# Kernel optimization log

Hardware: AMD Instinct MI355X
Metric: run time of the kernel (lower is better)

## Reference

```python
import jax, jax.numpy as jnp
import numpy as np

M0 = 0.3
R = 2
H = W = 64  # grid size from init_kwargs
N = H * W
B = 2


def _make_grid():
    # grid_by(lims=[[1,-1],[-1,1]], size=(64,64)): cartesian_prod of the two
    # linspaces, then columns swapped via index_select([1, 0]).
    a = jnp.linspace(1.0, -1.0, H)
    b = jnp.linspace(-1.0, 1.0, W)
    ga, gb = jnp.meshgrid(a, b, indexing='ij')
    cart = jnp.stack([ga, gb], axis=-1).reshape(N, 2)  # cartesian_prod order
    return cart[:, ::-1]  # swap columns -> [N, 2]


def setup_inputs() -> dict:
    key = jax.random.key(0)
    k1, k2 = jax.random.split(key)
    grid = _make_grid()
    # input points = grid + small jitter (avoids exactly-zero distances)
    inp = grid[None, :, :] + 0.05 * jax.random.normal(k1, (B, N, 2), dtype=jnp.float32)
    weight = jax.random.uniform(k2, (B, N), dtype=jnp.float32)
    return {"input": inp, "weight": weight, "grid": grid}


def reference(input, weight, grid):
    # --- brute-force KNN (r=2), k = N (full sort; equivalent to torch max_k path) ---
    # dist[b, j, i] = || grid_j - input_{b,i} ||_2   (note the .mT in torch knn)
    d2 = jnp.sum((grid[None, :, None, :] - input[:, None, :, :]) ** 2, axis=-1)  # [B,N,N]
    dist = jnp.sqrt(d2)
    order = jnp.argsort(dist, axis=-1)                       # ascending distance
    knn_dist = jnp.take_along_axis(dist, order, axis=-1)     # [B,N,N]
    knn_index = order                                        # indices into input points

    # --- weighted DTM ---
    weight_bound = M0 * jnp.sum(weight, axis=-1, keepdims=True)   # [B,1]
    wb = weight_bound[:, :, None]                                  # [B,1,1]
    # gather per-row weights of the sorted neighbors
    knn_weight = jax.vmap(lambda w, idx: w[idx])(weight, knn_index)  # [B,N,N]
    cum_knn_weight = jnp.cumsum(knn_weight, axis=-1)
    # searchsorted (left): first index where cumulative weight >= bound
    k_index = jnp.sum(cum_knn_weight < wb, axis=-1, keepdims=True)   # [B,N,1]
    k_index = jnp.minimum(k_index, N - 1)

    r_dist = knn_dist ** 2  # r == 2
    cum_dist = jnp.cumsum(r_dist * knn_weight, axis=-1)
    dtm_val = jnp.take_along_axis(
        cum_dist + r_dist * (wb - cum_knn_weight), k_index, axis=-1
    ).squeeze(-1)                                                    # [B,N]
    return jnp.sqrt(dtm_val / weight_bound)
```

## Files before the change

### kernel.cpp

```cpp
#include <hip/hip_runtime.h>
#include <math.h>

namespace {

constexpr int   kN       = 4096;
constexpr int   kThreads = 256;
constexpr int   kEPT     = kN / 64;
constexpr int   kGroups  = kEPT / 2;
constexpr int   kIters   = 9;
constexpr float kM0      = 0.3f;
constexpr float kS       = 2048.f;
constexpr float kRootS   = 45.25483399593904f;

typedef _Float16 h2 __attribute__((ext_vector_type(2)));

__device__ __forceinline__ float dppStep_(float x, int t) {
    return x + __builtin_bit_cast(float, t);
}
__device__ __forceinline__ float waveSumUniform(float x) {
    int xi;
    xi = __builtin_amdgcn_update_dpp(0, __builtin_bit_cast(int, x), 0x111, 0xf, 0xf, true);
    x  = dppStep_(x, xi);
    xi = __builtin_amdgcn_update_dpp(0, __builtin_bit_cast(int, x), 0x112, 0xf, 0xf, true);
    x  = dppStep_(x, xi);
    xi = __builtin_amdgcn_update_dpp(0, __builtin_bit_cast(int, x), 0x114, 0xf, 0xf, true);
    x  = dppStep_(x, xi);
    xi = __builtin_amdgcn_update_dpp(0, __builtin_bit_cast(int, x), 0x118, 0xf, 0xf, true);
    x  = dppStep_(x, xi);
    xi = __builtin_amdgcn_update_dpp(0, __builtin_bit_cast(int, x), 0x142, 0xa, 0xf, true);
    x  = dppStep_(x, xi);
    xi = __builtin_amdgcn_update_dpp(0, __builtin_bit_cast(int, x), 0x143, 0xc, 0xf, true);
    x  = dppStep_(x, xi);
    return __builtin_bit_cast(float, __builtin_amdgcn_readlane(__builtin_bit_cast(int, x), 63));
}

__device__ __forceinline__ h2 subClamp(h2 m, h2 d) {
    h2 r;
    asm("v_pk_add_f16 %0, %1, %2 neg_lo:[0,1] neg_hi:[0,1] clamp"
        : "=v"(r) : "v"(m), "v"(d));
    return r;
}

__global__ __launch_bounds__(kThreads, 4)
void dtm_kernel(const float* __restrict__ input,
                const float* __restrict__ weight,
                const float* __restrict__ grid,
                float* __restrict__ out,
                int nq) {
    const int lane = threadIdx.x & 63;
    const int wave = threadIdx.x >> 6;
    const int wglob = blockIdx.x * 4 + wave;
    const int b    = wglob >> 11;
    const int wid  = wglob & 2047;
    const int i0 = wid;
    const int i1 = wid + kN / 2;
    if (b * kN + i1 >= nq) return;

    const float sgxA = kRootS * grid[2 * i0], sgyA = kRootS * grid[2 * i0 + 1];
    const float sgxB = kRootS * grid[2 * i1], sgyB = kRootS * grid[2 * i1 + 1];
    const float4* inp4 = (const float4*)(input + (size_t)b * kN * 2);
    const float4* wgt4 = (const float4*)(weight + (size_t)b * kN);

    const h2 one2 = h2{(_Float16)1.f, (_Float16)1.f};

    h2 dA[kGroups], dB[kGroups], ws[kGroups];
    float wl = 0.f;
#pragma unroll
    for (int s = 0; s < kGroups / 2; ++s) {
        const int g = lane + 64 * s;
        const float4 wv = wgt4[g];
        const float4 pa = inp4[2 * g];
        const float4 pb = inp4[2 * g + 1];
        float dx, dy, e0, e1, e2, e3;
        dx = fmaf(-kRootS, pa.x, sgxA); dy = fmaf(-kRootS, pa.y, sgyA); e0 = fmaf(dy, dy, dx * dx);
        dx = fmaf(-kRootS, pa.z, sgxA); dy = fmaf(-kRootS, pa.w, sgyA); e1 = fmaf(dy, dy, dx * dx);
        dx = fmaf(-kRootS, pb.x, sgxA); dy = fmaf(-kRootS, pb.y, sgyA); e2 = fmaf(dy, dy, dx * dx);
        dx = fmaf(-kRootS, pb.z, sgxA); dy = fmaf(-kRootS, pb.w, sgyA); e3 = fmaf(dy, dy, dx * dx);
        dA[2 * s]     = h2{(_Float16)e0, (_Float16)e1};
        dA[2 * s + 1] = h2{(_Float16)e2, (_Float16)e3};
        dx = fmaf(-kRootS, pa.x, sgxB); dy = fmaf(-kRootS, pa.y, sgyB); e0 = fmaf(dy, dy, dx * dx);
        dx = fmaf(-kRootS, pa.z, sgxB); dy = fmaf(-kRootS, pa.w, sgyB); e1 = fmaf(dy, dy, dx * dx);
        dx = fmaf(-kRootS, pb.x, sgxB); dy = fmaf(-kRootS, pb.y, sgyB); e2 = fmaf(dy, dy, dx * dx);
        dx = fmaf(-kRootS, pb.z, sgxB); dy = fmaf(-kRootS, pb.w, sgyB); e3 = fmaf(dy, dy, dx * dx);
        dB[2 * s]     = h2{(_Float16)e0, (_Float16)e1};
        dB[2 * s + 1] = h2{(_Float16)e2, (_Float16)e3};
        ws[2 * s]     = h2{(_Float16)wv.x, (_Float16)wv.y};
        ws[2 * s + 1] = h2{(_Float16)wv.z, (_Float16)wv.w};
        wl = __builtin_amdgcn_fdot2(ws[2 * s],     one2, wl, false);
        wl = __builtin_amdgcn_fdot2(ws[2 * s + 1], one2, wl, false);
    }
    const float wb = kM0 * waveSumUniform(wl);

    float loA = 0.f, hiA = 32768.f, TloA = 0.f;
    float loB = 0.f, hiB = 32768.f, TloB = 0.f;
#pragma unroll 1
    for (int it = 0; it < kIters; ++it) {
        const float midA = 0.5f * (loA + hiA);
        const float midB = 0.5f * (loB + hiB);
        const _Float16 mAh = (_Float16)midA;
        const _Float16 mBh = (_Float16)midB;
        const h2 mA2 = h2{mAh, mAh};
        const h2 mB2 = h2{mBh, mBh};
        float a0 = 0.f, a1 = 0.f, b0 = 0.f, b1 = 0.f;
#pragma unroll
        for (int g = 0; g < kGroups; g += 2) {
            h2 tA0 = subClamp(mA2, dA[g]);
            h2 tA1 = subClamp(mA2, dA[g + 1]);
            h2 tB0 = subClamp(mB2, dB[g]);
            h2 tB1 = subClamp(mB2, dB[g + 1]);
            a0 = __builtin_amdgcn_fdot2(ws[g],     tA0, a0, false);
            a1 = __builtin_amdgcn_fdot2(ws[g + 1], tA1, a1, false);
            b0 = __builtin_amdgcn_fdot2(ws[g],     tB0, b0, false);
            b1 = __builtin_amdgcn_fdot2(ws[g + 1], tB1, b1, false);
        }
        const float TA = waveSumUniform(a0 + a1);
        const float TB = waveSumUniform(b0 + b1);
        if (TA >= wb) hiA = midA; else { loA = midA; TloA = TA; }
        if (TB >= wb) hiB = midB; else { loB = midB; TloB = TB; }
    }

    {
        const _Float16 lAh = (_Float16)loA;
        const _Float16 lBh = (_Float16)loB;
        const h2 lA2 = h2{lAh, lAh};
        const h2 lB2 = h2{lBh, lBh};
        float A0 = 0.f, A1 = 0.f, B0 = 0.f, B1 = 0.f;
#pragma unroll
        for (int g = 0; g < kGroups; g += 2) {
            const h2 tA0 = subClamp(lA2, dA[g]);
            const h2 tA1 = subClamp(lA2, dA[g + 1]);
            const h2 tB0 = subClamp(lB2, dB[g]);
            const h2 tB1 = subClamp(lB2, dB[g + 1]);
            const h2 pA0 = dA[g] * ws[g];
            const h2 pA1 = dA[g + 1] * ws[g + 1];
            const h2 pB0 = dB[g] * ws[g];
            const h2 pB1 = dB[g + 1] * ws[g + 1];
            A0 = __builtin_amdgcn_fdot2(pA0, tA0, A0, false);
            A1 = __builtin_amdgcn_fdot2(pA1, tA1, A1, false);
            B0 = __builtin_amdgcn_fdot2(pB0, tB0, B0, false);
            B1 = __builtin_amdgcn_fdot2(pB1, tB1, B1, false);
        }
        const float AA = waveSumUniform(A0 + A1);
        const float AB = waveSumUniform(B0 + B1);
        if (lane == 0) {
            const float dtmA = (AA + hiA * (wb - TloA)) * (1.f / kS);
            const float dtmB = (AB + hiB * (wb - TloB)) * (1.f / kS);
            float* ob = out + (size_t)b * kN;
            ob[i0] = sqrtf(fmaxf(dtmA, 0.f) / wb);
            ob[i1] = sqrtf(fmaxf(dtmB, 0.f) / wb);
        }
    }
}

}

extern "C" void kernel_launch(void* const* d_in, const int* in_sizes, int n_in,
                              void* d_out, int out_size, void* d_ws, size_t ws_size,
                              hipStream_t stream) {
    const float* input  = (const float*)d_in[0];
    const float* weight = (const float*)d_in[1];
    const float* grid   = (const float*)d_in[2];
    float* out = (float*)d_out;
    const int nq = out_size;
    const int blocks = (nq + 7) / 8;
    dtm_kernel<<<dim3(blocks), dim3(kThreads), 0, stream>>>(input, weight, grid, out, nq);
}
```

Baseline: 75.39 us.

## Seed bisection with an asymmetric split and adaptively stop refinement iterations

The bisection search for the threshold now begins with one evaluation at a seed value of 4096, which splits the range unevenly. It then runs 6 fixed iterations, followed by up to 3 extra iterations that run only while an interval is still wider than about 64, so uniform waves can exit early. The distance setup also switches to packed f32 FMA inline assembly, processing both query points per instruction. The aim is fewer full passes over the 64 fp16 distance registers per wave, at the cost of more branching and a possible accuracy difference when the seed lands badly.

Result: no change. 74.13 us (-1.7%).

```diff
diff --git a/kernel.cpp b/kernel.cpp
--- a/kernel.cpp
+++ b/kernel.cpp
@@ -3,16 +3,19 @@
 
 namespace {
 
-constexpr int   kN       = 4096;
-constexpr int   kThreads = 256;
-constexpr int   kEPT     = kN / 64;
-constexpr int   kGroups  = kEPT / 2;
-constexpr int   kIters   = 9;
-constexpr float kM0      = 0.3f;
-constexpr float kS       = 2048.f;
-constexpr float kRootS   = 45.25483399593904f;
+constexpr int   kN         = 4096;
+constexpr int   kThreads   = 256;
+constexpr int   kGroups    = 32;
+constexpr int   kItersMain = 6;
+constexpr float kM0        = 0.3f;
+constexpr float kS         = 2048.f;
+constexpr float kRootS     = 45.25483399593904f;
+constexpr float kSeed      = 4096.f;
+constexpr float kTop       = 32768.f;
 
 typedef _Float16 h2 __attribute__((ext_vector_type(2)));
+typedef float    f2 __attribute__((ext_vector_type(2)));
+typedef float    f4 __attribute__((ext_vector_type(4)));
 
 __device__ __forceinline__ float dppStep_(float x, int t) {
     return x + __builtin_bit_cast(float, t);
@@ -39,6 +42,44 @@
     asm("v_pk_add_f16 %0, %1, %2 neg_lo:[0,1] neg_hi:[0,1] clamp"
         : "=v"(r) : "v"(m), "v"(d));
     return r;
+}
+
+__device__ __forceinline__ f2 pk_fma_bx(f2 a, f2 p, f2 c) {
+    f2 d;
+    asm("v_pk_fma_f32 %0, %1, %2, %3 op_sel_hi:[1,0,1]"
+        : "=v"(d) : "v"(a), "v"(p), "v"(c));
+    return d;
+}
+__device__ __forceinline__ f2 pk_fma_by(f2 a, f2 p, f2 c) {
+    f2 d;
+    asm("v_pk_fma_f32 %0, %1, %2, %3 op_sel:[0,1,0] op_sel_hi:[1,1,1]"
+        : "=v"(d) : "v"(a), "v"(p), "v"(c));
+    return d;
+}
+__device__ __forceinline__ f2 pk_mul(f2 a, f2 b) {
+    f2 d; asm("v_pk_mul_f32 %0, %1, %2" : "=v"(d) : "v"(a), "v"(b)); return d;
+}
+__device__ __forceinline__ f2 pk_fma(f2 a, f2 b, f2 c) {
+    f2 d; asm("v_pk_fma_f32 %0, %1, %2, %3" : "=v"(d) : "v"(a), "v"(b), "v"(c)); return d;
+}
+
+__device__ __forceinline__ void evalT(const h2 (&dA)[kGroups], const h2 (&dB)[kGroups],
+                                      const h2 (&ws)[kGroups], h2 mA2, h2 mB2,
+                                      float& TA, float& TB) {
+    float a0 = 0.f, a1 = 0.f, b0 = 0.f, b1 = 0.f;
+#pragma unroll
+    for (int g = 0; g < kGroups; g += 2) {
+        h2 tA0 = subClamp(mA2, dA[g]);
+        h2 tA1 = subClamp(mA2, dA[g + 1]);
+        h2 tB0 = subClamp(mB2, dB[g]);
+        h2 tB1 = subClamp(mB2, dB[g + 1]);
+        a0 = __builtin_amdgcn_fdot2(ws[g],     tA0, a0, false);
+        a1 = __builtin_amdgcn_fdot2(ws[g + 1], tA1, a1, false);
+        b0 = __builtin_amdgcn_fdot2(ws[g],     tB0, b0, false);
+        b1 = __builtin_amdgcn_fdot2(ws[g + 1], tB1, b1, false);
+    }
+    TA = waveSumUniform(a0 + a1);
+    TB = waveSumUniform(b0 + b1);
 }
 
 __global__ __launch_bounds__(kThreads, 4)
@@ -58,65 +99,84 @@
 
     const float sgxA = kRootS * grid[2 * i0], sgyA = kRootS * grid[2 * i0 + 1];
     const float sgxB = kRootS * grid[2 * i1], sgyB = kRootS * grid[2 * i1 + 1];
-    const float4* inp4 = (const float4*)(input + (size_t)b * kN * 2);
-    const float4* wgt4 = (const float4*)(weight + (size_t)b * kN);
-
-    const h2 one2 = h2{(_Float16)1.f, (_Float16)1.f};
+    const f4* inp4 = (const f4*)(input + (size_t)b * kN * 2);
+    const f4* wgt4 = (const f4*)(weight + (size_t)b * kN);
+
+    const h2 one2  = h2{(_Float16)1.f, (_Float16)1.f};
+    const f2 negr2 = f2{-kRootS, -kRootS};
+    const f2 sgx2  = f2{sgxA, sgxB};
+    const f2 sgy2  = f2{sgyA, sgyB};
 
     h2 dA[kGroups], dB[kGroups], ws[kGroups];
     float wl = 0.f;
 #pragma unroll
     for (int s = 0; s < kGroups / 2; ++s) {
         const int g = lane + 64 * s;
-        const float4 wv = wgt4[g];
-        const float4 pa = inp4[2 * g];
-        const float4 pb = inp4[2 * g + 1];
-        float dx, dy, e0, e1, e2, e3;
-        dx = fmaf(-kRootS, pa.x, sgxA); dy = fmaf(-kRootS, pa.y, sgyA); e0 = fmaf(dy, dy, dx * dx);
-        dx = fmaf(-kRootS, pa.z, sgxA); dy = fmaf(-kRootS, pa.w, sgyA); e1 = fmaf(dy, dy, dx * dx);
-        dx = fmaf(-kRootS, pb.x, sgxA); dy = fmaf(-kRootS, pb.y, sgyA); e2 = fmaf(dy, dy, dx * dx);
-        dx = fmaf(-kRootS, pb.z, sgxA); dy = fmaf(-kRootS, pb.w, sgyA); e3 = fmaf(dy, dy, dx * dx);
-        dA[2 * s]     = h2{(_Float16)e0, (_Float16)e1};
-        dA[2 * s + 1] = h2{(_Float16)e2, (_Float16)e3};
-        dx = fmaf(-kRootS, pa.x, sgxB); dy = fmaf(-kRootS, pa.y, sgyB); e0 = fmaf(dy, dy, dx * dx);
-        dx = fmaf(-kRootS, pa.z, sgxB); dy = fmaf(-kRootS, pa.w, sgyB); e1 = fmaf(dy, dy, dx * dx);
-        dx = fmaf(-kRootS, pb.x, sgxB); dy = fmaf(-kRootS, pb.y, sgyB); e2 = fmaf(dy, dy, dx * dx);
-        dx = fmaf(-kRootS, pb.z, sgxB); dy = fmaf(-kRootS, pb.w, sgyB); e3 = fmaf(dy, dy, dx * dx);
-        dB[2 * s]     = h2{(_Float16)e0, (_Float16)e1};
-        dB[2 * s + 1] = h2{(_Float16)e2, (_Float16)e3};
-        ws[2 * s]     = h2{(_Float16)wv.x, (_Float16)wv.y};
-        ws[2 * s + 1] = h2{(_Float16)wv.z, (_Float16)wv.w};
+        const f4 wv  = wgt4[g];
+        const f4 pa4 = inp4[2 * g];
+        const f4 pb4 = inp4[2 * g + 1];
+        const f2 p0 = __builtin_shufflevector(pa4, pa4, 0, 1);
+        const f2 p1 = __builtin_shufflevector(pa4, pa4, 2, 3);
+        const f2 p2 = __builtin_shufflevector(pb4, pb4, 0, 1);
+        const f2 p3 = __builtin_shufflevector(pb4, pb4, 2, 3);
+        f2 dx, dy, q0, q1, q2, q3;
+        dx = pk_fma_bx(negr2, p0, sgx2); dy = pk_fma_by(negr2, p0, sgy2);
+        q0 = pk_fma(dy, dy, pk_mul(dx, dx));
+        dx = pk_fma_bx(negr2, p1, sgx2); dy = pk_fma_by(negr2, p1, sgy2);
+        q1 = pk_fma(dy, dy, pk_mul(dx, dx));
+        dx = pk_fma_bx(negr2, p2, sgx2); dy = pk_fma_by(negr2, p2, sgy2);
+        q2 = pk_fma(dy, dy, pk_mul(dx, dx));
+        dx = pk_fma_bx(negr2, p3, sgx2); dy = pk_fma_by(negr2, p3, sgy2);
+        q3 = pk_fma(dy, dy, pk_mul(dx, dx));
+        dA[2 * s]     = h2{(_Float16)q0[0], (_Float16)q1[0]};
+        dA[2 * s + 1] = h2{(_Float16)q2[0], (_Float16)q3[0]};
+        dB[2 * s]     = h2{(_Float16)q0[1], (_Float16)q1[1]};
+        dB[2 * s + 1] = h2{(_Float16)q2[1], (_Float16)q3[1]};
+        ws[2 * s]     = h2{(_Float16)wv[0], (_Float16)wv[1]};
+        ws[2 * s + 1] = h2{(_Float16)wv[2], (_Float16)wv[3]};
         wl = __builtin_amdgcn_fdot2(ws[2 * s],     one2, wl, false);
         wl = __builtin_amdgcn_fdot2(ws[2 * s + 1], one2, wl, false);
     }
     const float wb = kM0 * waveSumUniform(wl);
 
-    float loA = 0.f, hiA = 32768.f, TloA = 0.f;
-    float loB = 0.f, hiB = 32768.f, TloB = 0.f;
+    float loA, hiA, TloA, loB, hiB, TloB;
+    {
+        const _Float16 sh = (_Float16)kSeed;
+        const h2 s2 = h2{sh, sh};
+        float TA, TB;
+        evalT(dA, dB, ws, s2, s2, TA, TB);
+        if (TA >= wb) { loA = 0.f;   hiA = kSeed; TloA = 0.f; }
+        else          { loA = kSeed; hiA = kTop;  TloA = TA;  }
+        if (TB >= wb) { loB = 0.f;   hiB = kSeed; TloB = 0.f; }
+        else          { loB = kSeed; hiB = kTop;  TloB = TB;  }
+    }
+
 #pragma unroll 1
-    for (int it = 0; it < kIters; ++it) {
+    for (int it = 0; it < kItersMain; ++it) {
         const float midA = 0.5f * (loA + hiA);
         const float midB = 0.5f * (loB + hiB);
         const _Float16 mAh = (_Float16)midA;
         const _Float16 mBh = (_Float16)midB;
-        const h2 mA2 = h2{mAh, mAh};
-        const h2 mB2 = h2{mBh, mBh};
-        float a0 = 0.f, a1 = 0.f, b0 = 0.f, b1 = 0.f;
-#pragma unroll
-        for (int g = 0; g < kGroups; g += 2) {
-            h2 tA0 = subClamp(mA2, dA[g]);
-            h2 tA1 = subClamp(mA2, dA[g + 1]);
-            h2 tB0 = subClamp(mB2, dB[g]);
-            h2 tB1 = subClamp(mB2, dB[g + 1]);
-            a0 = __builtin_amdgcn_fdot2(ws[g],     tA0, a0, false);
-            a1 = __builtin_amdgcn_fdot2(ws[g + 1], tA1, a1, false);
-            b0 = __builtin_amdgcn_fdot2(ws[g],     tB0, b0, false);
-            b1 = __builtin_amdgcn_fdot2(ws[g + 1], tB1, b1, false);
-        }
-        const float TA = waveSumUniform(a0 + a1);
-        const float TB = waveSumUniform(b0 + b1);
+        float TA, TB;
+        evalT(dA, dB, ws, h2{mAh, mAh}, h2{mBh, mBh}, TA, TB);
         if (TA >= wb) hiA = midA; else { loA = midA; TloA = TA; }
         if (TB >= wb) hiB = midB; else { loB = midB; TloB = TB; }
+    }
+
+#pragma unroll 1
+    for (int e = 0; e < 3; ++e) {
+        const bool wideA = (hiA - loA) > 64.5f;
+        const bool wideB = (hiB - loB) > 64.5f;
+        if (!wideA && !wideB) break;
+        float midA = 0.5f * (loA + hiA);
+        float midB = 0.5f * (loB + hiB);
+        const _Float16 mAh = (_Float16)midA;
+        const _Float16 mBh = (_Float16)midB;
+        midA = (float)mAh; midB = (float)mBh;
+        float TA, TB;
+        evalT(dA, dB, ws, h2{mAh, mAh}, h2{mBh, mBh}, TA, TB);
+        if (wideA) { if (TA >= wb) hiA = midA; else { loA = midA; TloA = TA; } }
+        if (wideB) { if (TB >= wb) hiB = midB; else { loB = midB; TloB = TB; } }
     }
 
     {
```
